# Performance work log

Measured on AMD Instinct MI355X. Metric: run time of the kernel, lower is better.

## Reference

```python
import jax, jax.numpy as jnp
import numpy as np

B, S, D, H = 2, 2048, 1024, 16
HD = D // H
SCALE = HD ** -0.5
NEG = -1e30


def setup_inputs() -> dict:
    key = jax.random.key(0)
    ks = jax.random.split(key, 10)
    w = lambda k: jax.random.normal(k, (D, D), dtype=jnp.float32) * 0.02
    b = lambda k: jax.random.normal(k, (D,), dtype=jnp.float32) * 0.01
    hidden_states = jax.random.normal(ks[0], (B, S, D), dtype=jnp.float32)
    document_ids = jnp.sort(jax.random.randint(ks[1], (S,), 0, 16))
    return {
        'hidden_states': hidden_states,
        'wq': w(ks[2]), 'bq': b(ks[3]),
        'wk': w(ks[4]), 'bk': b(ks[5]),
        'wv': w(ks[6]), 'bv': b(ks[7]),
        'wo': w(ks[8]), 'bo': b(ks[9]),
        'document_ids': document_ids,
    }


def reference(hidden_states, wq, bq, wk, bk, wv, bv, wo, bo, document_ids):
    # projections (nn.Linear: x @ W.T + b)
    q = (hidden_states @ wq.T + bq).reshape(B, S, H, HD)
    k = (hidden_states @ wk.T + bk).reshape(B, S, H, HD)
    v = (hidden_states @ wv.T + bv).reshape(B, S, H, HD)
    # document-block mask: attend only within same document
    mask = document_ids[:, None] == document_ids[None, :]  # [S, S]
    scores = jnp.einsum('bqhd,bkhd->bhqk', q, k) * SCALE
    scores = jnp.where(mask[None, None], scores, NEG)
    attn = jax.nn.softmax(scores, axis=-1)
    out = jnp.einsum('bhqk,bkhd->bqhd', attn, v).reshape(B, S, D)
    return out @ wo.T + bo
```

## Files before the change

### kernel.cpp

```cpp
#include <hip/hip_runtime.h>
#include <hip/hip_bf16.h>
#include <math.h>

#define B 2
#define S 2048
#define D 1024
#define H 16
#define HD 64
#define SCALE 0.125f
#define NEGBIG -1e30f
#define TQ 64

typedef _Float16 f16;
typedef _Float16 f16x8 __attribute__((ext_vector_type(8)));
typedef _Float16 f16x4 __attribute__((ext_vector_type(4)));
typedef float f32x4  __attribute__((ext_vector_type(4)));

__device__ __forceinline__ void gl_lds16(const void* g, void* l) {
    __builtin_amdgcn_global_load_lds(
        (const __attribute__((address_space(1))) unsigned int*)g,
        (__attribute__((address_space(3))) unsigned int*)l, 16, 0, 0);
}

__global__ __launch_bounds__(256) void convx_k(const float4* __restrict__ src,
                                               f16x8* __restrict__ dst, int n8) {
    int i = blockIdx.x * blockDim.x + threadIdx.x;
    if (i >= n8) return;
    float4 a = src[2 * i], b = src[2 * i + 1];
    f16x8 h;
    h[0] = (f16)a.x; h[1] = (f16)a.y; h[2] = (f16)a.z; h[3] = (f16)a.w;
    h[4] = (f16)b.x; h[5] = (f16)b.y; h[6] = (f16)b.z; h[7] = (f16)b.w;
    dst[i] = h;
}

__global__ __launch_bounds__(256) void convw_k(
    const float4* __restrict__ wq, const float4* __restrict__ wk,
    const float4* __restrict__ wv, const float4* __restrict__ wo,
    f16x8* __restrict__ wqkv, f16x8* __restrict__ woh, int n8) {
    int i = blockIdx.x * blockDim.x + threadIdx.x;
    if (i >= 4 * n8) return;
    int id = i / n8;
    int j = i - id * n8;
    const float4* src = (id == 0) ? wq : (id == 1) ? wk : (id == 2) ? wv : wo;
    f16x8* dst = (id < 3) ? (wqkv + (size_t)id * n8 + j) : (woh + j);
    float4 a = src[2 * j], b = src[2 * j + 1];
    f16x8 h;
    h[0] = (f16)a.x; h[1] = (f16)a.y; h[2] = (f16)a.z; h[3] = (f16)a.w;
    h[4] = (f16)b.x; h[5] = (f16)b.y; h[6] = (f16)b.z; h[7] = (f16)b.w;
    *dst = h;
}

__global__ void docbounds_k(const int* __restrict__ doc, int* __restrict__ dstart,
                            int* __restrict__ dend) {
    int i = blockIdx.x * blockDim.x + threadIdx.x;
    if (i >= S) return;
    int v = doc[i];
    int lo = 0, hi = S;
    while (lo < hi) { int mid = (lo + hi) >> 1; if (doc[mid] < v) lo = mid + 1; else hi = mid; }
    dstart[i] = lo;
    lo = 0; hi = S;
    while (lo < hi) { int mid = (lo + hi) >> 1; if (doc[mid] <= v) lo = mid + 1; else hi = mid; }
    dend[i] = lo;
}

__global__ __launch_bounds__(256) void qkv_mfma_k(
    const f16* __restrict__ xh, const f16* __restrict__ wqkv,
    const float* __restrict__ bq, const float* __restrict__ bk,
    const float* __restrict__ bv,
    f16* __restrict__ Qh, f16* __restrict__ Kh, f16* __restrict__ Vth)
{
    __shared__ union {
        struct { f16 Ah[128 * 32]; f16 Bh[128 * 32]; } s;
        f16 tr[64 * 136];
    } lds;

    const int which = blockIdx.z;
    const f16* Bhg = wqkv + (size_t)which * D * D;

    const int tid = threadIdx.x;
    const int w = tid >> 6, ln = tid & 63;
    const int wm = (w & 1) * 64, wn = (w >> 1) * 64;
    const int lc = ln & 15, quad = ln >> 4;
    const int srow = ln >> 2, slot = ln & 3;
    const int m0 = blockIdx.y * 128, n0 = blockIdx.x * 128;

    int a_off[4], b_off[4];
    #pragma unroll
    for (int t = 0; t < 4; t++) {
        int am = wm + t * 16 + lc;
        a_off[t] = am * 32 + ((quad ^ ((am >> 1) & 3)) * 8);
        int bn = wn + t * 16 + lc;
        b_off[t] = bn * 32 + ((quad ^ ((bn >> 1) & 3)) * 8);
    }

    f32x4 acc[4][4];
    #pragma unroll
    for (int i = 0; i < 4; i++)
        #pragma unroll
        for (int j = 0; j < 4; j++) acc[i][j] = (f32x4){0.f, 0.f, 0.f, 0.f};

    for (int k0 = 0; k0 < 1024; k0 += 32) {
        #pragma unroll
        for (int half = 0; half < 2; half++) {
            int rl = half * 64 + w * 16 + srow;
            int q = slot ^ ((rl >> 1) & 3);
            size_t ga = (size_t)(m0 + rl) * 1024 + k0 + q * 8;
            size_t gb = (size_t)(n0 + rl) * 1024 + k0 + q * 8;
            int lofs = (half * 64 + w * 16) * 32;
            gl_lds16(xh + ga, lds.s.Ah + lofs);
            gl_lds16(Bhg + gb, lds.s.Bh + lofs);
        }
        __syncthreads();

        f16x8 ah[4], bh[4];
        #pragma unroll
        for (int t = 0; t < 4; t++) {
            ah[t] = *(const f16x8*)&lds.s.Ah[a_off[t]];
            bh[t] = *(const f16x8*)&lds.s.Bh[b_off[t]];
        }
        #pragma unroll
        for (int mt = 0; mt < 4; mt++)
            #pragma unroll
            for (int nt = 0; nt < 4; nt++)
                acc[mt][nt] = __builtin_amdgcn_mfma_f32_16x16x32_f16(ah[mt], bh[nt], acc[mt][nt], 0, 0, 0);
        __syncthreads();
    }

    if (which < 2) {
        const float* bias = (which == 0) ? bq : bk;
        #pragma unroll
        for (int nt = 0; nt < 4; nt++) {
            int col = n0 + wn + nt * 16 + lc;
            float bv_ = bias[col];
            int h = col >> 6, hd = col & 63;
            #pragma unroll
            for (int mt = 0; mt < 4; mt++) {
                #pragma unroll
                for (int r = 0; r < 4; r++) {
                    int m = m0 + wm + mt * 16 + quad * 4 + r;
                    int bbm = m >> 11, s = m & (S - 1);
                    float val = acc[mt][nt][r] + bv_;
                    if (which == 0) val *= SCALE;
                    size_t idx = (((size_t)(bbm * H + h) * S) + s) * HD + hd;
                    ((which == 0) ? Qh : Kh)[idx] = (f16)val;
                }
            }
        }
    } else {
        const int bb = m0 >> 11;
        const int sbase = m0 & (S - 1);
        #pragma unroll
        for (int pass = 0; pass < 2; pass++) {
            if ((w >> 1) == pass) {
                #pragma unroll
                for (int nt = 0; nt < 4; nt++) {
                    int colp = nt * 16 + lc;
                    float bv_ = bv[n0 + pass * 64 + colp];
                    #pragma unroll
                    for (int mt = 0; mt < 4; mt++) {
                        f16x4 v;
                        #pragma unroll
                        for (int r = 0; r < 4; r++) v[r] = (f16)(acc[mt][nt][r] + bv_);
                        *(f16x4*)&lds.tr[colp * 136 + wm + mt * 16 + quad * 4] = v;
                    }
                }
            }
            __syncthreads();
            #pragma unroll
            for (int p2 = 0; p2 < 4; p2++) {
                int chunk = tid + p2 * 256;
                int colp = chunk >> 4;
                int oct = chunk & 15;
                f16x8 v = *(const f16x8*)&lds.tr[colp * 136 + oct * 8];
                int vcol = n0 + pass * 64 + colp;
                int h = vcol >> 6, hd = vcol & 63;
                size_t idx = (((size_t)(bb * H + h) * HD) + hd) * S + sbase + oct * 8;
                *(f16x8*)(Vth + idx) = v;
            }
            __syncthreads();
        }
    }
}

__global__ __launch_bounds__(256) void out_mfma_k(
    const f16* __restrict__ oh, const f16* __restrict__ wh,
    const float* __restrict__ bias, float* __restrict__ Y)
{
    __shared__ f16 Ah[128 * 32], Bh[128 * 32];
    const int tid = threadIdx.x;
    const int w = tid >> 6, ln = tid & 63;
    const int wm = (w & 1) * 64, wn = (w >> 1) * 64;
    const int lc = ln & 15, quad = ln >> 4;
    const int srow = ln >> 2, slot = ln & 3;
    const int m0 = blockIdx.y * 128, n0 = blockIdx.x * 128;

    int a_off[4], b_off[4];
    #pragma unroll
    for (int t = 0; t < 4; t++) {
        int am = wm + t * 16 + lc;
        a_off[t] = am * 32 + ((quad ^ ((am >> 1) & 3)) * 8);
        int bn = wn + t * 16 + lc;
        b_off[t] = bn * 32 + ((quad ^ ((bn >> 1) & 3)) * 8);
    }

    f32x4 acc[4][4];
    #pragma unroll
    for (int i = 0; i < 4; i++)
        #pragma unroll
        for (int j = 0; j < 4; j++) acc[i][j] = (f32x4){0.f, 0.f, 0.f, 0.f};

    for (int k0 = 0; k0 < 1024; k0 += 32) {
        #pragma unroll
        for (int half = 0; half < 2; half++) {
            int rl = half * 64 + w * 16 + srow;
            int q = slot ^ ((rl >> 1) & 3);
            size_t ga = (size_t)(m0 + rl) * 1024 + k0 + q * 8;
            size_t gb = (size_t)(n0 + rl) * 1024 + k0 + q * 8;
            int lofs = (half * 64 + w * 16) * 32;
            gl_lds16(oh + ga, Ah + lofs);
            gl_lds16(wh + gb, Bh + lofs);
        }
        __syncthreads();

        f16x8 ah[4], bh[4];
        #pragma unroll
        for (int t = 0; t < 4; t++) {
            ah[t] = *(const f16x8*)&Ah[a_off[t]];
            bh[t] = *(const f16x8*)&Bh[b_off[t]];
        }
        #pragma unroll
        for (int mt = 0; mt < 4; mt++)
            #pragma unroll
            for (int nt = 0; nt < 4; nt++)
                acc[mt][nt] = __builtin_amdgcn_mfma_f32_16x16x32_f16(ah[mt], bh[nt], acc[mt][nt], 0, 0, 0);
        __syncthreads();
    }

    #pragma unroll
    for (int nt = 0; nt < 4; nt++) {
        int col = n0 + wn + nt * 16 + lc;
        float bv_ = bias[col];
        #pragma unroll
        for (int mt = 0; mt < 4; mt++) {
            #pragma unroll
            for (int r = 0; r < 4; r++) {
                int m = m0 + wm + mt * 16 + quad * 4 + r;
                Y[(size_t)m * D + col] = acc[mt][nt][r] + bv_;
            }
        }
    }
}

__global__ __launch_bounds__(256) void attn3_k(
    const f16* __restrict__ Qh, const f16* __restrict__ Kh,
    const f16* __restrict__ Vth,
    const int* __restrict__ dstart, const int* __restrict__ dend,
    f16* __restrict__ Ohi)
{
    const int qt = blockIdx.x, h = blockIdx.y, b = blockIdx.z;
    const int q0 = qt * TQ;
    const size_t bh  = ((size_t)b * H + h) * S;
    const size_t bhv = ((size_t)b * H + h) * HD;

    const int tid = threadIdx.x;
    const int w = tid >> 6, ln = tid & 63;
    const int lc = ln & 15, quad = ln >> 4;

    __shared__ f16 VtHs[64 * 64];
    __shared__ float Ps[4][16 * 64];
    __shared__ int sb[TQ], se[TQ];

    if (tid < TQ) { sb[tid] = dstart[q0 + tid]; se[tid] = dend[q0 + tid]; }

    const size_t qrow = bh + q0 + w * 16 + lc;
    f16x8 qfh[2];
    #pragma unroll
    for (int ks = 0; ks < 2; ks++)
        qfh[ks] = *(const f16x8*)(Qh + qrow * HD + ks * 32 + quad * 8);
    __syncthreads();

    int row_st[4], row_en[4];
    #pragma unroll
    for (int r = 0; r < 4; r++) {
        row_st[r] = sb[w * 16 + quad * 4 + r];
        row_en[r] = se[w * 16 + quad * 4 + r];
    }
    const int kstart = sb[0] & ~63;
    const int kend   = se[TQ - 1];

    f32x4 o[4];
    #pragma unroll
    for (int nt = 0; nt < 4; nt++) o[nt] = (f32x4){0.f, 0.f, 0.f, 0.f};
    f32x4 m_i = (f32x4){NEGBIG, NEGBIG, NEGBIG, NEGBIG};
    f32x4 l_i = (f32x4){0.f, 0.f, 0.f, 0.f};

    for (int j0 = kstart; j0 < kend; j0 += 64) {
        __syncthreads();
        #pragma unroll
        for (int p = 0; p < 2; p++) {
            int idx = tid + p * 256;
            int dim = idx >> 3, g = idx & 7;
            int slot = g ^ (dim & 7);
            *(uint4*)&VtHs[dim * 64 + slot * 8] =
                *(const uint4*)(Vth + (bhv + dim) * S + j0 + g * 8);
        }

        f16x8 kfh[4][2];
        #pragma unroll
        for (int t = 0; t < 4; t++) {
            size_t krow = (bh + j0 + t * 16 + lc) * HD;
            #pragma unroll
            for (int ks = 0; ks < 2; ks++)
                kfh[t][ks] = *(const f16x8*)(Kh + krow + ks * 32 + quad * 8);
        }
        __syncthreads();

        f32x4 sc[4];
        #pragma unroll
        for (int t = 0; t < 4; t++) {
            f32x4 a = (f32x4){0.f, 0.f, 0.f, 0.f};
            #pragma unroll
            for (int ks = 0; ks < 2; ks++)
                a = __builtin_amdgcn_mfma_f32_16x16x32_f16(qfh[ks], kfh[t][ks], a, 0, 0, 0);
            int key = j0 + t * 16 + lc;
            #pragma unroll
            for (int r = 0; r < 4; r++) {
                bool valid = (key >= row_st[r]) && (key < row_en[r]);
                sc[t][r] = valid ? a[r] : NEGBIG;
            }
        }

        f32x4 mx = sc[0];
        #pragma unroll
        for (int t = 1; t < 4; t++)
            #pragma unroll
            for (int r = 0; r < 4; r++) mx[r] = fmaxf(mx[r], sc[t][r]);
        #pragma unroll
        for (int off = 1; off <= 8; off <<= 1)
            #pragma unroll
            for (int r = 0; r < 4; r++) mx[r] = fmaxf(mx[r], __shfl_xor(mx[r], off, 64));

        f32x4 m_new, alpha;
        #pragma unroll
        for (int r = 0; r < 4; r++) {
            m_new[r] = fmaxf(m_i[r], mx[r]);
            alpha[r] = __expf(m_i[r] - m_new[r]);
        }

        f32x4 psum = (f32x4){0.f, 0.f, 0.f, 0.f};
        f32x4 pv[4];
        #pragma unroll
        for (int t = 0; t < 4; t++) {
            #pragma unroll
            for (int r = 0; r < 4; r++) {
                float p = __expf(sc[t][r] - m_new[r]);
                p = (sc[t][r] < -5e29f) ? 0.f : p;
                pv[t][r] = p;
                psum[r] += p;
            }
        }
        #pragma unroll
        for (int off = 1; off <= 8; off <<= 1)
            #pragma unroll
            for (int r = 0; r < 4; r++) psum[r] += __shfl_xor(psum[r], off, 64);

        #pragma unroll
        for (int r = 0; r < 4; r++) {
            l_i[r] = l_i[r] * alpha[r] + psum[r];
            m_i[r] = m_new[r];
        }
        #pragma unroll
        for (int nt = 0; nt < 4; nt++)
            #pragma unroll
            for (int r = 0; r < 4; r++) o[nt][r] *= alpha[r];

        #pragma unroll
        for (int t = 0; t < 4; t++) {
            int g = 2 * t + (lc >> 3);
            #pragma unroll
            for (int r = 0; r < 4; r++) {
                int q = quad * 4 + r;
                Ps[w][q * 64 + ((g ^ (q & 7)) * 8) + (lc & 7)] = pv[t][r];
            }
        }
        __syncthreads();

        #pragma unroll
        for (int ks = 0; ks < 2; ks++) {
            int gp = ks * 4 + quad;
            const float* prow = &Ps[w][lc * 64 + ((gp ^ (lc & 7)) * 8)];
            f16x8 ph;
            #pragma unroll
            for (int j = 0; j < 8; j++) ph[j] = (f16)prow[j];
            #pragma unroll
            for (int nt = 0; nt < 4; nt++) {
                int dim = nt * 16 + lc;
                int slot = gp ^ (dim & 7);
                f16x8 vh = *(const f16x8*)&VtHs[dim * 64 + slot * 8];
                o[nt] = __builtin_amdgcn_mfma_f32_16x16x32_f16(ph, vh, o[nt], 0, 0, 0);
            }
        }
    }

    f32x4 inv;
    #pragma unroll
    for (int r = 0; r < 4; r++) inv[r] = 1.f / l_i[r];
    #pragma unroll
    for (int nt = 0; nt < 4; nt++) {
        int dim = nt * 16 + lc;
        #pragma unroll
        for (int r = 0; r < 4; r++) {
            int q = q0 + w * 16 + quad * 4 + r;
            float val = o[nt][r] * inv[r];
            size_t idx = ((size_t)(b * S + q)) * D + h * 64 + dim;
            Ohi[idx] = (f16)val;
        }
    }
}

extern "C" void kernel_launch(void* const* d_in, const int* in_sizes, int n_in,
                              void* d_out, int out_size, void* d_ws, size_t ws_size,
                              hipStream_t stream) {
    const float* hs = (const float*)d_in[0];
    const float* wq = (const float*)d_in[1];
    const float* bq = (const float*)d_in[2];
    const float* wk = (const float*)d_in[3];
    const float* bk = (const float*)d_in[4];
    const float* wv = (const float*)d_in[5];
    const float* bv = (const float*)d_in[6];
    const float* wo = (const float*)d_in[7];
    const float* bo = (const float*)d_in[8];
    const int*  doc = (const int*)d_in[9];
    float* out = (float*)d_out;

    const size_t NE = (size_t)B * S * D;
    const size_t NW = (size_t)D * D;
    f16* xh   = (f16*)d_ws;
    f16* Qhb  = xh + NE;
    f16* Khb  = Qhb + NE;
    f16* Vth  = Khb + NE;
    f16* wqkv = Vth + NE;
    f16* woh  = wqkv + 3 * NW;
    int* dstart = (int*)(woh + NW);
    int* dend = dstart + S;

    docbounds_k<<<(S + 255) / 256, 256, 0, stream>>>(doc, dstart, dend);
    convx_k<<<(int)(NE / 8 / 256), 256, 0, stream>>>((const float4*)hs, (f16x8*)xh, (int)(NE / 8));
    convw_k<<<(int)(4 * NW / 8 / 256), 256, 0, stream>>>(
        (const float4*)wq, (const float4*)wk, (const float4*)wv, (const float4*)wo,
        (f16x8*)wqkv, (f16x8*)woh, (int)(NW / 8));

    qkv_mfma_k<<<dim3(D / 128, (B * S) / 128, 3), 256, 0, stream>>>(
        xh, wqkv, bq, bk, bv, Qhb, Khb, Vth);
    attn3_k<<<dim3(S / TQ, H, B), 256, 0, stream>>>(
        Qhb, Khb, Vth, dstart, dend, xh);
    out_mfma_k<<<dim3(D / 128, (B * S) / 128), 256, 0, stream>>>(xh, woh, bo, out);
}
```

Baseline: 213.2 us.

## Merge prep kernels and make attention waves independent with per-wave key ranges

Fuses the three preprocessing launches (x conversion, weight conversion, document bounds) into one kernel. The attention kernel now lets each wave loop over only the key range its own 16 query rows need, instead of the whole block's range. It drops the block-wide barriers and the shared V tile: V fragments are read straight from global memory, and P goes through a per-wave double-buffered, padded LDS area protected by a wave-level fence. This removes block synchronisation and extra key tiles for waves whose rows lie in a single document, but it loses V reuse across the four waves, which may raise global and L2 traffic.

```diff
diff --git a/kernel.cpp b/kernel.cpp
--- a/kernel.cpp
+++ b/kernel.cpp
@@ -9,7 +9,11 @@
 #define HD 64
 #define SCALE 0.125f
 #define NEGBIG -1e30f
-#define TQ 64
+
+#define NE 4194304
+#define NW 1048576
+#define NE8 524288
+#define NW8 131072
 
 typedef _Float16 f16;
 typedef _Float16 f16x8 __attribute__((ext_vector_type(8)));
@@ -22,45 +26,48 @@
         (__attribute__((address_space(3))) unsigned int*)l, 16, 0, 0);
 }
 
-__global__ __launch_bounds__(256) void convx_k(const float4* __restrict__ src,
-                                               f16x8* __restrict__ dst, int n8) {
-    int i = blockIdx.x * blockDim.x + threadIdx.x;
-    if (i >= n8) return;
-    float4 a = src[2 * i], b = src[2 * i + 1];
-    f16x8 h;
-    h[0] = (f16)a.x; h[1] = (f16)a.y; h[2] = (f16)a.z; h[3] = (f16)a.w;
-    h[4] = (f16)b.x; h[5] = (f16)b.y; h[6] = (f16)b.z; h[7] = (f16)b.w;
-    dst[i] = h;
-}
-
-__global__ __launch_bounds__(256) void convw_k(
+__device__ __forceinline__ void wave_lds_fence() {
+    __builtin_amdgcn_wave_barrier();
+    __builtin_amdgcn_s_waitcnt(0xC07F);
+    __builtin_amdgcn_wave_barrier();
+}
+
+__global__ __launch_bounds__(256) void prep_k(
+    const float4* __restrict__ hs,
     const float4* __restrict__ wq, const float4* __restrict__ wk,
     const float4* __restrict__ wv, const float4* __restrict__ wo,
-    f16x8* __restrict__ wqkv, f16x8* __restrict__ woh, int n8) {
+    const int* __restrict__ doc,
+    f16x8* __restrict__ xh, f16x8* __restrict__ wqkv, f16x8* __restrict__ woh,
+    int* __restrict__ dstart, int* __restrict__ dend)
+{
     int i = blockIdx.x * blockDim.x + threadIdx.x;
-    if (i >= 4 * n8) return;
-    int id = i / n8;
-    int j = i - id * n8;
-    const float4* src = (id == 0) ? wq : (id == 1) ? wk : (id == 2) ? wv : wo;
-    f16x8* dst = (id < 3) ? (wqkv + (size_t)id * n8 + j) : (woh + j);
-    float4 a = src[2 * j], b = src[2 * j + 1];
-    f16x8 h;
-    h[0] = (f16)a.x; h[1] = (f16)a.y; h[2] = (f16)a.z; h[3] = (f16)a.w;
-    h[4] = (f16)b.x; h[5] = (f16)b.y; h[6] = (f16)b.z; h[7] = (f16)b.w;
-    *dst = h;
-}
-
-__global__ void docbounds_k(const int* __restrict__ doc, int* __restrict__ dstart,
-                            int* __restrict__ dend) {
-    int i = blockIdx.x * blockDim.x + threadIdx.x;
-    if (i >= S) return;
-    int v = doc[i];
-    int lo = 0, hi = S;
-    while (lo < hi) { int mid = (lo + hi) >> 1; if (doc[mid] < v) lo = mid + 1; else hi = mid; }
-    dstart[i] = lo;
-    lo = 0; hi = S;
-    while (lo < hi) { int mid = (lo + hi) >> 1; if (doc[mid] <= v) lo = mid + 1; else hi = mid; }
-    dend[i] = lo;
+    if (i < NE8 + 4 * NW8) {
+        const float4* src;
+        f16x8* dst;
+        if (i < NE8) { src = hs + 2 * (size_t)i; dst = xh + i; }
+        else {
+            int j = i - NE8;
+            int id = j / NW8, jj = j - id * NW8;
+            src = ((id == 0) ? wq : (id == 1) ? wk : (id == 2) ? wv : wo) + 2 * (size_t)jj;
+            dst = (id < 3) ? (wqkv + (size_t)id * NW8 + jj) : (woh + jj);
+        }
+        float4 a = src[0], b = src[1];
+        f16x8 h;
+        h[0] = (f16)a.x; h[1] = (f16)a.y; h[2] = (f16)a.z; h[3] = (f16)a.w;
+        h[4] = (f16)b.x; h[5] = (f16)b.y; h[6] = (f16)b.z; h[7] = (f16)b.w;
+        *dst = h;
+    } else {
+        int s = i - (NE8 + 4 * NW8);
+        if (s < S) {
+            int v = doc[s];
+            int lo = 0, hi = S;
+            while (lo < hi) { int mid = (lo + hi) >> 1; if (doc[mid] < v) lo = mid + 1; else hi = mid; }
+            dstart[s] = lo;
+            lo = 0; hi = S;
+            while (lo < hi) { int mid = (lo + hi) >> 1; if (doc[mid] <= v) lo = mid + 1; else hi = mid; }
+            dend[s] = lo;
+        }
+    }
 }
 
 __global__ __launch_bounds__(256) void qkv_mfma_k(
@@ -251,42 +258,36 @@
     }
 }
 
-__global__ __launch_bounds__(256) void attn3_k(
+__global__ __launch_bounds__(256) void attn4_k(
     const f16* __restrict__ Qh, const f16* __restrict__ Kh,
     const f16* __restrict__ Vth,
     const int* __restrict__ dstart, const int* __restrict__ dend,
     f16* __restrict__ Ohi)
 {
     const int qt = blockIdx.x, h = blockIdx.y, b = blockIdx.z;
-    const int q0 = qt * TQ;
-    const size_t bh  = ((size_t)b * H + h) * S;
-    const size_t bhv = ((size_t)b * H + h) * HD;
-
     const int tid = threadIdx.x;
     const int w = tid >> 6, ln = tid & 63;
     const int lc = ln & 15, quad = ln >> 4;
-
-    __shared__ f16 VtHs[64 * 64];
-    __shared__ float Ps[4][16 * 64];
-    __shared__ int sb[TQ], se[TQ];
-
-    if (tid < TQ) { sb[tid] = dstart[q0 + tid]; se[tid] = dend[q0 + tid]; }
-
-    const size_t qrow = bh + q0 + w * 16 + lc;
-    f16x8 qfh[2];
+    const int q0 = qt * 64 + w * 16;
+    const size_t bh  = ((size_t)b * H + h) * S;
+    const size_t bhv = ((size_t)b * H + h) * HD;
+
+    __shared__ float Ps[4][2][16 * 65];
+
+    int row_st[4], row_en[4];
+    #pragma unroll
+    for (int r = 0; r < 4; r++) {
+        row_st[r] = dstart[q0 + quad * 4 + r];
+        row_en[r] = dend[q0 + quad * 4 + r];
+    }
+    const int kstart = dstart[q0] & ~63;
+    const int kend   = dend[q0 + 15];
+
+    const size_t qrow = bh + q0 + lc;
+    f16x8 qf[2];
     #pragma unroll
     for (int ks = 0; ks < 2; ks++)
-        qfh[ks] = *(const f16x8*)(Qh + qrow * HD + ks * 32 + quad * 8);
-    __syncthreads();
-
-    int row_st[4], row_en[4];
-    #pragma unroll
-    for (int r = 0; r < 4; r++) {
-        row_st[r] = sb[w * 16 + quad * 4 + r];
-        row_en[r] = se[w * 16 + quad * 4 + r];
-    }
-    const int kstart = sb[0] & ~63;
-    const int kend   = se[TQ - 1];
+        qf[ks] = *(const f16x8*)(Qh + qrow * HD + ks * 32 + quad * 8);
 
     f32x4 o[4];
     #pragma unroll
@@ -294,26 +295,18 @@
     f32x4 m_i = (f32x4){NEGBIG, NEGBIG, NEGBIG, NEGBIG};
     f32x4 l_i = (f32x4){0.f, 0.f, 0.f, 0.f};
 
-    for (int j0 = kstart; j0 < kend; j0 += 64) {
-        __syncthreads();
-        #pragma unroll
-        for (int p = 0; p < 2; p++) {
-            int idx = tid + p * 256;
-            int dim = idx >> 3, g = idx & 7;
-            int slot = g ^ (dim & 7);
-            *(uint4*)&VtHs[dim * 64 + slot * 8] =
-                *(const uint4*)(Vth + (bhv + dim) * S + j0 + g * 8);
-        }
-
-        f16x8 kfh[4][2];
+    int it = 0;
+    for (int j0 = kstart; j0 < kend; j0 += 64, it ^= 1) {
+        float* ps = &Ps[w][it][0];
+
+        f16x8 kf[4][2];
         #pragma unroll
         for (int t = 0; t < 4; t++) {
             size_t krow = (bh + j0 + t * 16 + lc) * HD;
             #pragma unroll
             for (int ks = 0; ks < 2; ks++)
-                kfh[t][ks] = *(const f16x8*)(Kh + krow + ks * 32 + quad * 8);
-        }
-        __syncthreads();
+                kf[t][ks] = *(const f16x8*)(Kh + krow + ks * 32 + quad * 8);
+        }
 
         f32x4 sc[4];
         #pragma unroll
@@ -321,7 +314,7 @@
             f32x4 a = (f32x4){0.f, 0.f, 0.f, 0.f};
             #pragma unroll
             for (int ks = 0; ks < 2; ks++)
-                a = __builtin_amdgcn_mfma_f32_16x16x32_f16(qfh[ks], kfh[t][ks], a, 0, 0, 0);
+                a = __builtin_amdgcn_mfma_f32_16x16x32_f16(qf[ks], kf[t][ks], a, 0, 0, 0);
             int key = j0 + t * 16 + lc;
             #pragma unroll
             for (int r = 0; r < 4; r++) {
@@ -380,23 +373,23 @@
             #pragma unroll
             for (int r = 0; r < 4; r++) {
                 int q = quad * 4 + r;
-                Ps[w][q * 64 + ((g ^ (q & 7)) * 8) + (lc & 7)] = pv[t][r];
-            }
-        }
-        __syncthreads();
+                ps[q * 65 + ((g ^ (q & 7)) * 8) + (lc & 7)] = pv[t][r];
+            }
+        }
+
+        wave_lds_fence();
 
         #pragma unroll
         for (int ks = 0; ks < 2; ks++) {
             int gp = ks * 4 + quad;
-            const float* prow = &Ps[w][lc * 64 + ((gp ^ (lc & 7)) * 8)];
+            const float* prow = &ps[lc * 65 + ((gp ^ (lc & 7)) * 8)];
             f16x8 ph;
             #pragma unroll
             for (int j = 0; j < 8; j++) ph[j] = (f16)prow[j];
             #pragma unroll
             for (int nt = 0; nt < 4; nt++) {
                 int dim = nt * 16 + lc;
-                int slot = gp ^ (dim & 7);
-                f16x8 vh = *(const f16x8*)&VtHs[dim * 64 + slot * 8];
+                f16x8 vh = *(const f16x8*)(Vth + (bhv + dim) * S + j0 + gp * 8);
                 o[nt] = __builtin_amdgcn_mfma_f32_16x16x32_f16(ph, vh, o[nt], 0, 0, 0);
             }
         }
@@ -410,7 +403,7 @@
         int dim = nt * 16 + lc;
         #pragma unroll
         for (int r = 0; r < 4; r++) {
-            int q = q0 + w * 16 + quad * 4 + r;
+            int q = q0 + quad * 4 + r;
             float val = o[nt][r] * inv[r];
             size_t idx = ((size_t)(b * S + q)) * D + h * 64 + dim;
             Ohi[idx] = (f16)val;
@@ -433,26 +426,23 @@
     const int*  doc = (const int*)d_in[9];
     float* out = (float*)d_out;
 
-    const size_t NE = (size_t)B * S * D;
-    const size_t NW = (size_t)D * D;
     f16* xh   = (f16*)d_ws;
     f16* Qhb  = xh + NE;
     f16* Khb  = Qhb + NE;
     f16* Vth  = Khb + NE;
     f16* wqkv = Vth + NE;
-    f16* woh  = wqkv + 3 * NW;
+    f16* woh  = wqkv + 3 * (size_t)NW;
     int* dstart = (int*)(woh + NW);
     int* dend = dstart + S;
 
-    docbounds_k<<<(S + 255) / 256, 256, 0, stream>>>(doc, dstart, dend);
-    convx_k<<<(int)(NE / 8 / 256), 256, 0, stream>>>((const float4*)hs, (f16x8*)xh, (int)(NE / 8));
-    convw_k<<<(int)(4 * NW / 8 / 256), 256, 0, stream>>>(
-        (const float4*)wq, (const float4*)wk, (const float4*)wv, (const float4*)wo,
-        (f16x8*)wqkv, (f16x8*)woh, (int)(NW / 8));
+    prep_k<<<(NE8 + 4 * NW8 + S + 255) / 256, 256, 0, stream>>>(
+        (const float4*)hs, (const float4*)wq, (const float4*)wk,
+        (const float4*)wv, (const float4*)wo, doc,
+        (f16x8*)xh, (f16x8*)wqkv, (f16x8*)woh, dstart, dend);
 
     qkv_mfma_k<<<dim3(D / 128, (B * S) / 128, 3), 256, 0, stream>>>(
         xh, wqkv, bq, bk, bv, Qhb, Khb, Vth);
-    attn3_k<<<dim3(S / TQ, H, B), 256, 0, stream>>>(
+    attn4_k<<<dim3(S / 64, H, B), 256, 0, stream>>>(
         Qhb, Khb, Vth, dstart, dend, xh);
     out_mfma_k<<<dim3(D / 128, (B * S) / 128), 256, 0, stream>>>(xh, woh, bo, out);
 }
```

After: 201.3 us. 1.06x faster.
